# Performance work log

Hardware: AMD Instinct MI355X
Metric: run time of the kernel (lower is better)

Reference implementation:

```python
import jax, jax.numpy as jnp
import numpy as np

B = 4; RESO = 64; VIT = 16; PAD = 0.1; TRI_C = 64; IMG_C = 1280
INNER = 128; OUT_C = 64; HEADS = 8; NIMG = 5
N_TRI = 3 * RESO * RESO  # 12288 triplane locations


def pos_enc(d_model, length):
    pos = jnp.arange(length, dtype=jnp.float32)[:, None]
    div = jnp.exp(jnp.arange(0, d_model, 2, dtype=jnp.float32) * (-np.log(10000.0) / d_model))
    pe = jnp.zeros((length, d_model), jnp.float32)
    pe = pe.at[:, 0::2].set(jnp.sin(pos * div)).at[:, 1::2].set(jnp.cos(pos * div))
    return pe


def triplane_coords():
    ar = jnp.arange(RESO, dtype=jnp.float32)
    A, Bm = jnp.meshgrid(ar, ar, indexing='xy')  # matches torch indexing='xy'
    half = jnp.full_like(A, (RESO - 1) / 2.0)
    xz = jnp.stack([A, half, Bm], -1)
    xy = jnp.stack([A, Bm, half], -1)
    yz = jnp.stack([half, A, Bm], -1)
    c = jnp.concatenate([xz, xy, yz], 0).reshape(-1, 3)
    c = c / (RESO - 1)
    return (c - 0.5) * 2.0 * (1.0 + PAD + 1e-05)  # [N_TRI, 3]


def trilinear_sample(vol, grid):
    # vol [B,C,D,H,W]; grid [B,M,3] in [-1,1] as (x->W, y->H, z->D); align_corners=True
    Bv, C, D, H, W = vol.shape
    gx, gy, gz = grid[..., 0], grid[..., 1], grid[..., 2]
    ix = (gx + 1.0) * 0.5 * (W - 1)
    iy = (gy + 1.0) * 0.5 * (H - 1)
    iz = (gz + 1.0) * 0.5 * (D - 1)
    x0 = jnp.floor(ix); y0 = jnp.floor(iy); z0 = jnp.floor(iz)
    wx = ix - x0; wy = iy - y0; wz = iz - z0
    x0i = jnp.clip(x0.astype(jnp.int32), 0, W - 1); x1i = jnp.clip(x0i + 1, 0, W - 1)
    y0i = jnp.clip(y0.astype(jnp.int32), 0, H - 1); y1i = jnp.clip(y0i + 1, 0, H - 1)
    z0i = jnp.clip(z0.astype(jnp.int32), 0, D - 1); z1i = jnp.clip(z0i + 1, 0, D - 1)
    vf = vol.reshape(Bv, C, D * H * W)
    def g(zi, yi, xi):
        idx = (zi * H + yi) * W + xi  # [B,M]
        return jnp.take_along_axis(vf, idx[:, None, :], axis=2)  # [B,C,M]
    out = 0.0
    for zi, wz_ in ((z0i, 1.0 - wz), (z1i, wz)):
        for yi, wy_ in ((y0i, 1.0 - wy), (y1i, wy)):
            for xi, wx_ in ((x0i, 1.0 - wx), (x1i, wx)):
                out = out + g(zi, yi, xi) * (wz_ * wy_ * wx_)[:, None, :]
    return out  # [B,C,M]


def _forward(triplane_feat, image_feat, proj_mat, k_w, k_b, q_w, q_b, v_w, v_b,
             in_w, in_b, out_w, out_b, conv_w, conv_b, valid_frames):
    Bb, n_img = image_feat.shape[0], image_feat.shape[1]
    img = image_feat[:, :, 1:, :]  # drop CLS -> [B,n,256,1280]
    pe_img = pos_enc(INNER, VIT * VIT)  # [256,128]
    kimg = img @ k_w.T + k_b + pe_img
    vimg = img @ v_w.T + v_b + pe_img
    kv = jnp.concatenate([kimg, vimg], -1)  # [B,n,256,2E]
    vol = kv.reshape(Bb, n_img, VIT, VIT, 2 * INNER).transpose(0, 4, 1, 2, 3)  # [B,2E,D,H,W]

    coords = triplane_coords()
    homo = jnp.concatenate([coords, jnp.ones((N_TRI, 1), jnp.float32)], -1)  # [N,4]
    cin = jnp.einsum('nc,bjkc->bjnk', homo, proj_mat)  # == homo @ proj^T
    x = cin[..., 0] / cin[..., 2] / (224.0 - 1)
    y = cin[..., 1] / cin[..., 2] / (224.0 - 1)
    xy = (jnp.stack([x, y], -1) - 0.5) * 2.0
    gi = (jnp.arange(n_img, dtype=jnp.float32) / (n_img - 1) - 0.5) * 2.0
    gi = jnp.broadcast_to(gi[None, :, None, None], (Bb, n_img, N_TRI, 1))
    grid = jnp.clip(jnp.concatenate([xy, gi], -1), -1.0, 1.0)  # [B,n,N,3]

    samp = trilinear_sample(vol, grid.reshape(Bb, n_img * N_TRI, 3))
    samp = samp.reshape(Bb, 2 * INNER, n_img, N_TRI)
    kk = samp[:, :INNER].transpose(0, 3, 2, 1)  # [B,N,n,E]
    vv = samp[:, INNER:].transpose(0, 3, 2, 1)

    tq = triplane_feat.reshape(Bb, TRI_C, N_TRI).transpose(0, 2, 1)  # b (h w) c
    q = tq @ q_w.T + q_b + pos_enc(INNER, N_TRI)

    E, dh = INNER, INNER // HEADS
    Wq, Wk, Wv = in_w[:E], in_w[E:2 * E], in_w[2 * E:]
    bq, bk, bv = in_b[:E], in_b[E:2 * E], in_b[2 * E:]
    qp = (q @ Wq.T + bq).reshape(Bb, N_TRI, HEADS, dh)
    kp = (kk @ Wk.T + bk).reshape(Bb, N_TRI, n_img, HEADS, dh)
    vp = (vv @ Wv.T + bv).reshape(Bb, N_TRI, n_img, HEADS, dh)
    scores = jnp.einsum('bnhd,bnjhd->bnhj', qp, kp) / np.sqrt(dh).astype(np.float32)
    attn = jax.nn.softmax(scores, axis=-1)
    o = jnp.einsum('bnhj,bnjhd->bnhd', attn, vp).reshape(Bb, N_TRI, E)
    o = o @ out_w.T + out_b  # [B,N,E]

    t = o.transpose(0, 2, 1).reshape(Bb, E, 3 * RESO, RESO)
    return jnp.einsum('bchw,oc->bohw', t, conv_w) + conv_b[None, :, None, None]


def setup_inputs() -> dict:
    key = jax.random.key(0)
    ks = jax.random.split(key, 16)
    s = 0.02
    pm = jax.random.normal(ks[2], (B, NIMG, 4, 4), jnp.float32)
    proj = pm * 30.0  # pixel-scale projection rows
    zrow = jnp.concatenate([pm[..., 2, :3] * 0.05, 3.0 + 0.5 * jnp.abs(pm[..., 2, 3:4])], -1)
    proj_mat = proj.at[..., 2, :].set(zrow)  # positive depth, safe division
    return {
        'triplane_feat': jax.random.normal(ks[0], (B, TRI_C, 3 * RESO, RESO), jnp.float32),
        'image_feat': jax.random.normal(ks[1], (B, NIMG, VIT * VIT + 1, IMG_C), jnp.float32),
        'proj_mat': proj_mat,
        'valid_frames': jnp.ones((B, NIMG), jnp.int32),
        'k_w': jax.random.normal(ks[3], (INNER, IMG_C), jnp.float32) * s,
        'k_b': jnp.zeros((INNER,), jnp.float32),
        'q_w': jax.random.normal(ks[4], (INNER, TRI_C), jnp.float32) * s,
        'q_b': jnp.zeros((INNER,), jnp.float32),
        'v_w': jax.random.normal(ks[5], (INNER, IMG_C), jnp.float32) * s,
        'v_b': jnp.zeros((INNER,), jnp.float32),
        'in_w': jax.random.normal(ks[6], (3 * INNER, INNER), jnp.float32) * s,
        'in_b': jnp.zeros((3 * INNER,), jnp.float32),
        'out_w': jax.random.normal(ks[7], (INNER, INNER), jnp.float32) * s,
        'out_b': jnp.zeros((INNER,), jnp.float32),
        'conv_w': jax.random.normal(ks[8], (OUT_C, INNER), jnp.float32) * s,
        'conv_b': jnp.zeros((OUT_C,), jnp.float32),
    }


def reference(triplane_feat, image_feat, proj_mat, valid_frames, k_w, k_b, q_w, q_b,
              v_w, v_b, in_w, in_b, out_w, out_b, conv_w, conv_b):
    return _forward(triplane_feat, image_feat, proj_mat, k_w, k_b, q_w, q_b, v_w, v_b,
                    in_w, in_b, out_w, out_b, conv_w, conv_b, valid_frames)
```

## Files before the change

kernel.cpp:

```cpp
#include <hip/hip_runtime.h>
#include <math.h>

#define NTRI 12288

#define OFF_WT    0u
#define OFF_PEKV  327680u
#define OFF_CQWT  393216u
#define OFF_PEQ   401408u
#define OFF_W2T   1974272u
#define OFF_B2    1982464u
#define OFF_INWT  1982528u
#define OFF_KVPV  2031680u
#define OFF_GTAB  3342400u

typedef short short8 __attribute__((ext_vector_type(8)));
typedef float f32x4 __attribute__((ext_vector_type(4)));

__device__ __forceinline__ unsigned short f2bf(float f) {
  unsigned u = __float_as_uint(f);
  return (unsigned short)((u + 0x7fff + ((u >> 16) & 1)) >> 16);
}
__device__ __forceinline__ float bflo(unsigned u) {
  return __uint_as_float(u << 16);
}
__device__ __forceinline__ float bfhi(unsigned u) {
  return __uint_as_float(u & 0xffff0000u);
}

__global__ __launch_bounds__(256) void k_inwT(const float* __restrict__ in_w,
                                              float* __restrict__ inwT) {
  int idx = blockIdx.x * 256 + threadIdx.x;
  int r = idx >> 7, m = idx & 127;
  inwT[m * 384 + r] = in_w[idx];
}

__global__ __launch_bounds__(256) void k_pre(const float* __restrict__ inwT,
    const float* __restrict__ k_w, const float* __restrict__ v_w,
    const float* __restrict__ k_b, const float* __restrict__ v_b,
    const float* __restrict__ in_b, const float* __restrict__ q_w,
    const float* __restrict__ q_b, const float* __restrict__ conv_w,
    const float* __restrict__ out_w, const float* __restrict__ out_b,
    const float* __restrict__ conv_b, const float* __restrict__ proj,
    unsigned short* __restrict__ wTc, float* __restrict__ pekv,
    float* __restrict__ cqwT, float* __restrict__ peq,
    float* __restrict__ w2t, float* __restrict__ b2,
    float4* __restrict__ gtab) {
  __shared__ float spe8[8][128];
  int bb = blockIdx.x;
  int t = threadIdx.x;

  if (bb < 1280) {
    int i = bb, c = t;
    const float* src = (c < 128) ? k_w : v_w;
    float acc = 0.f;
    for (int m = 0; m < 128; ++m)
      acc += inwT[m * 384 + 128 + c] * src[m * 1280 + i];
    wTc[(size_t)c * 1280 + i] = f2bf(acc);
  } else if (bb < 1536) {
    int p = bb - 1280;
    if (t < 128) {
      float dv = (float)exp(-(double)(t & ~1) * (9.210340371976184 / 128.0));
      float arg = (float)p * dv;
      spe8[0][t] = (t & 1) ? cosf(arg) : sinf(arg);
    }
    __syncthreads();
    const float* bias = (t < 128) ? k_b : v_b;
    float acc = 0.f;
    for (int m = 0; m < 128; ++m)
      acc += inwT[m * 384 + 128 + t] * (bias[m] + spe8[0][m]);
    pekv[p * 256 + t] = acc + in_b[128 + t];
  } else if (bb < 1568) {
    int idx = (bb - 1536) * 256 + t;
    int k = idx >> 7, c = idx & 127;
    float acc = 0.f;
    for (int m = 0; m < 128; ++m)
      acc += inwT[m * 384 + c] * q_w[m * 64 + k];
    cqwT[idx] = acc;
  } else if (bb < 3104) {
    int n8 = (bb - 1568) * 8;
    for (int it = 0; it < 4; ++it) {
      int e = it * 256 + t;
      int nn = e >> 7, m = e & 127;
      float dv = (float)exp(-(double)(m & ~1) * (9.210340371976184 / 128.0));
      float arg = (float)(n8 + nn) * dv;
      spe8[nn][m] = q_b[m] + ((m & 1) ? cosf(arg) : sinf(arg));
    }
    __syncthreads();
    int c = t & 127, z = t >> 7;
    float a0 = 0, a1 = 0, a2 = 0, a3 = 0;
    for (int m = 0; m < 128; ++m) {
      float w = inwT[m * 384 + c];
      a0 += w * spe8[z * 4 + 0][m];
      a1 += w * spe8[z * 4 + 1][m];
      a2 += w * spe8[z * 4 + 2][m];
      a3 += w * spe8[z * 4 + 3][m];
    }
    float bbv = in_b[c];
    peq[(n8 + z * 4 + 0) * 128 + c] = a0 + bbv;
    peq[(n8 + z * 4 + 1) * 128 + c] = a1 + bbv;
    peq[(n8 + z * 4 + 2) * 128 + c] = a2 + bbv;
    peq[(n8 + z * 4 + 3) * 128 + c] = a3 + bbv;
  } else if (bb < 3137) {
    int idx = (bb - 3104) * 256 + t;
    if (idx < 8192) {
      int c = idx >> 6, oc = idx & 63;
      float acc = 0.f;
      for (int m = 0; m < 128; ++m)
        acc += conv_w[oc * 128 + m] * out_w[m * 128 + c];
      w2t[c * 64 + oc] = acc;
    } else if (idx < 8256) {
      int oc = idx - 8192;
      float acc = 0.f;
      for (int m = 0; m < 128; ++m)
        acc += conv_w[oc * 128 + m] * out_b[m];
      b2[oc] = acc + conv_b[oc];
    }
  } else {
    int idx = (bb - 3137) * 256 + t;
    int n = idx % NTRI;
    int bj = idx / NTRI;
    int plane = n >> 12, rem = n & 4095;
    float fa = (float)(rem & 63), fb = (float)(rem >> 6);
    float cx, cy, cz;
    if (plane == 0)      { cx = fa;    cy = 31.5f; cz = fb; }
    else if (plane == 1) { cx = fa;    cy = fb;    cz = 31.5f; }
    else                 { cx = 31.5f; cy = fa;    cz = fb; }
    const float s2 = 2.20002f;
    cx = (cx / 63.0f - 0.5f) * s2;
    cy = (cy / 63.0f - 0.5f) * s2;
    cz = (cz / 63.0f - 0.5f) * s2;
    const float* P = &proj[bj * 16];
    float d0 = cx * P[0] + cy * P[1] + cz * P[2] + P[3];
    float d1 = cx * P[4] + cy * P[5] + cz * P[6] + P[7];
    float d2 = cx * P[8] + cy * P[9] + cz * P[10] + P[11];
    float x = d0 / d2 / 223.0f;
    float y = d1 / d2 / 223.0f;
    float gx = fminf(fmaxf((x - 0.5f) * 2.0f, -1.0f), 1.0f);
    float gy = fminf(fmaxf((y - 0.5f) * 2.0f, -1.0f), 1.0f);
    float ix = (gx + 1.0f) * 7.5f, iy = (gy + 1.0f) * 7.5f;
    float fx = floorf(ix), fy = floorf(iy);
    float wx = ix - fx, wy = iy - fy;
    int x0 = (int)fx; x0 = x0 < 0 ? 0 : (x0 > 15 ? 15 : x0);
    int y0 = (int)fy; y0 = y0 < 0 ? 0 : (y0 > 15 ? 15 : y0);
    int x1 = x0 + 1 > 15 ? 15 : x0 + 1;
    int y1 = y0 + 1 > 15 ? 15 : y0 + 1;
    int pack = x0 | (x1 << 8) | (y0 << 16) | (y1 << 24);
    gtab[idx] = make_float4(wx, wy, __int_as_float(pack), 0.f);
  }
}

#define LDA 72
__global__ __launch_bounds__(256) void k_kv(const float* __restrict__ img,
    const unsigned short* __restrict__ wTc, const float* __restrict__ pekv,
    unsigned short* __restrict__ kv16) {
  __shared__ unsigned short sA[32 * LDA];
  __shared__ unsigned short sB[64 * LDA];
  int t = threadIdx.x;
  int gm = blockIdx.x >> 2;
  int gn = blockIdx.x & 3;
  int r0 = gm * 32, c0 = gn * 64;
  int lane = t & 63, w = t >> 6;
  int wm = w & 1, wn = w >> 1;
  int lrow = lane & 15, quad = lane >> 4;
  int srow = t >> 3, schunk = t & 7;
  int bj = gm >> 3;
  f32x4 acc0 = {0,0,0,0}, acc1 = {0,0,0,0};

  for (int kt = 0; kt < 20; ++kt) {
    int k0 = kt * 64;
    __syncthreads();
    {
      const float4* s = (const float4*)&img[(size_t)(r0 + srow + bj + 1) * 1280 + k0 + schunk * 8];
      float4 v0 = s[0], v1 = s[1];
      short8 av;
      av[0] = (short)f2bf(v0.x); av[1] = (short)f2bf(v0.y);
      av[2] = (short)f2bf(v0.z); av[3] = (short)f2bf(v0.w);
      av[4] = (short)f2bf(v1.x); av[5] = (short)f2bf(v1.y);
      av[6] = (short)f2bf(v1.z); av[7] = (short)f2bf(v1.w);
      *(short8*)&sA[srow * LDA + schunk * 8] = av;
      *(short8*)&sB[srow * LDA + schunk * 8] =
          *(const short8*)&wTc[(size_t)(c0 + srow) * 1280 + k0 + schunk * 8];
      *(short8*)&sB[(srow + 32) * LDA + schunk * 8] =
          *(const short8*)&wTc[(size_t)(c0 + srow + 32) * 1280 + k0 + schunk * 8];
    }
    __syncthreads();
#pragma unroll
    for (int kk = 0; kk < 2; ++kk) {
      int kof = kk * 32 + quad * 8;
      short8 a  = *(const short8*)&sA[(wm * 16 + lrow) * LDA + kof];
      short8 b0 = *(const short8*)&sB[(wn * 32 + lrow) * LDA + kof];
      short8 b1 = *(const short8*)&sB[(wn * 32 + 16 + lrow) * LDA + kof];
      acc0 = __builtin_amdgcn_mfma_f32_16x16x32_bf16(a, b0, acc0, 0, 0, 0);
      acc1 = __builtin_amdgcn_mfma_f32_16x16x32_bf16(a, b1, acc1, 0, 0, 0);
    }
  }
  f32x4 accs[2] = {acc0, acc1};
#pragma unroll
  for (int ni = 0; ni < 2; ++ni)
#pragma unroll
    for (int r = 0; r < 4; ++r) {
      int grow = r0 + wm * 16 + quad * 4 + r;
      int gcol = c0 + wn * 32 + ni * 16 + lrow;
      kv16[(size_t)grow * 256 + gcol] =
          f2bf(accs[ni][r] + pekv[(grow & 255) * 256 + gcol]);
    }
}

__global__ __launch_bounds__(256, 2) void k_main(const float* __restrict__ tri,
    const float* __restrict__ cqwT, const float* __restrict__ peq,
    const float* __restrict__ w2t, const float* __restrict__ b2,
    const unsigned short* __restrict__ kv16, const float4* __restrict__ gtab,
    float* __restrict__ outp) {
  __shared__ float sQP[32 * 132];
  __shared__ float sBuf[32 * 132];
  float* sTQ = sBuf;
  float* sO2 = sBuf;
  int t = threadIdx.x;
  int lane = t & 63, w = t >> 6;
  int b = blockIdx.x / 384;
  int n0 = (blockIdx.x % 384) * 32;

  for (int it = 0; it < 8; ++it) {
    int e = it * 256 + t;
    int k = e >> 5, pt = e & 31;
    sTQ[k * 36 + pt] = tri[(size_t)(b * 64 + k) * NTRI + n0 + pt];
  }
  __syncthreads();

  {
    int c4 = (t & 31) * 4;
    int p4 = (t >> 5) * 4;
    const float* cw = cqwT + c4;
    float4 A0 = {0,0,0,0}, A1 = {0,0,0,0}, A2 = {0,0,0,0}, A3 = {0,0,0,0};
#pragma unroll 4
    for (int k = 0; k < 64; ++k) {
      float4 wv = *(const float4*)(cw + k * 128);
      float4 aq = *(const float4*)&sTQ[k * 36 + p4];
      A0.x += aq.x * wv.x; A0.y += aq.x * wv.y; A0.z += aq.x * wv.z; A0.w += aq.x * wv.w;
      A1.x += aq.y * wv.x; A1.y += aq.y * wv.y; A1.z += aq.y * wv.z; A1.w += aq.y * wv.w;
      A2.x += aq.z * wv.x; A2.y += aq.z * wv.y; A2.z += aq.z * wv.z; A2.w += aq.z * wv.w;
      A3.x += aq.w * wv.x; A3.y += aq.w * wv.y; A3.z += aq.w * wv.z; A3.w += aq.w * wv.w;
    }
    float4 acc[4] = {A0, A1, A2, A3};
#pragma unroll
    for (int pp = 0; pp < 4; ++pp) {
      float4 pe = *(const float4*)&peq[(size_t)(n0 + p4 + pp) * 128 + c4];
      float4 r;
      r.x = acc[pp].x + pe.x; r.y = acc[pp].y + pe.y;
      r.z = acc[pp].z + pe.z; r.w = acc[pp].w + pe.w;
      *(float4*)&sQP[(p4 + pp) * 132 + c4] = r;
    }
  }
  __syncthreads();

  {
    int sub = lane & 31, half = lane >> 5, c4 = sub * 4;
    const unsigned short* Vb = kv16 + (size_t)b * 5 * 65536;
    const float4* gbase = &gtab[(size_t)(b * 5) * NTRI];
    for (int s = 0; s < 4; ++s) {
      int pt = s * 8 + w * 2 + half;
      int n = n0 + pt;
      float4 qp4 = *(const float4*)&sQP[pt * 132 + c4];
      float4 gp[5];
#pragma unroll
      for (int j = 0; j < 5; ++j) gp[j] = gbase[(size_t)j * NTRI + n];
      float4 vst[5];
      float sc[5];
#pragma unroll
      for (int j = 0; j < 5; ++j) {
        int pack = __float_as_int(gp[j].z);
        int x0 = pack & 255, x1 = (pack >> 8) & 255;
        int y0 = (pack >> 16) & 255, y1 = (pack >> 24) & 255;
        float wx = gp[j].x, wy = gp[j].y;
        const unsigned short* r0 = Vb + j * 65536 + y0 * 4096;
        const unsigned short* r1 = Vb + j * 65536 + y1 * 4096;
        int i0 = x0 * 256 + c4, i1 = x1 * 256 + c4;
        uint2 K00 = *(const uint2*)(r0 + i0), K01 = *(const uint2*)(r0 + i1);
        uint2 K10 = *(const uint2*)(r1 + i0), K11 = *(const uint2*)(r1 + i1);
        uint2 V00 = *(const uint2*)(r0 + i0 + 128), V01 = *(const uint2*)(r0 + i1 + 128);
        uint2 V10 = *(const uint2*)(r1 + i0 + 128), V11 = *(const uint2*)(r1 + i1 + 128);
        float w00 = (1.f - wx) * (1.f - wy), w01 = wx * (1.f - wy);
        float w10 = (1.f - wx) * wy, w11 = wx * wy;
        float4 kc, vc;
        kc.x = bflo(K00.x) * w00 + bflo(K01.x) * w01 + bflo(K10.x) * w10 + bflo(K11.x) * w11;
        kc.y = bfhi(K00.x) * w00 + bfhi(K01.x) * w01 + bfhi(K10.x) * w10 + bfhi(K11.x) * w11;
        kc.z = bflo(K00.y) * w00 + bflo(K01.y) * w01 + bflo(K10.y) * w10 + bflo(K11.y) * w11;
        kc.w = bfhi(K00.y) * w00 + bfhi(K01.y) * w01 + bfhi(K10.y) * w10 + bfhi(K11.y) * w11;
        vc.x = bflo(V00.x) * w00 + bflo(V01.x) * w01 + bflo(V10.x) * w10 + bflo(V11.x) * w11;
        vc.y = bfhi(V00.x) * w00 + bfhi(V01.x) * w01 + bfhi(V10.x) * w10 + bfhi(V11.x) * w11;
        vc.z = bflo(V00.y) * w00 + bflo(V01.y) * w01 + bflo(V10.y) * w10 + bflo(V11.y) * w11;
        vc.w = bfhi(V00.y) * w00 + bfhi(V01.y) * w01 + bfhi(V10.y) * w10 + bfhi(V11.y) * w11;
        vst[j] = vc;
        float pa = qp4.x * kc.x + qp4.y * kc.y + qp4.z * kc.z + qp4.w * kc.w;
        pa += __shfl_xor(pa, 1);
        pa += __shfl_xor(pa, 2);
        sc[j] = pa * 0.25f;
      }
      float mx = fmaxf(fmaxf(fmaxf(sc[0], sc[1]), fmaxf(sc[2], sc[3])), sc[4]);
      float e0 = expf(sc[0] - mx), e1 = expf(sc[1] - mx), e2 = expf(sc[2] - mx);
      float e3 = expf(sc[3] - mx), e4 = expf(sc[4] - mx);
      float inv = 1.0f / (e0 + e1 + e2 + e3 + e4);
      float4 oa;
      oa.x = (e0 * vst[0].x + e1 * vst[1].x + e2 * vst[2].x + e3 * vst[3].x + e4 * vst[4].x) * inv;
      oa.y = (e0 * vst[0].y + e1 * vst[1].y + e2 * vst[2].y + e3 * vst[3].y + e4 * vst[4].y) * inv;
      oa.z = (e0 * vst[0].z + e1 * vst[1].z + e2 * vst[2].z + e3 * vst[3].z + e4 * vst[4].z) * inv;
      oa.w = (e0 * vst[0].w + e1 * vst[1].w + e2 * vst[2].w + e3 * vst[3].w + e4 * vst[4].w) * inv;
      *(float4*)&sO2[pt * 132 + c4] = oa;
    }
  }
  __syncthreads();

  {
    int oc4 = (t & 15) * 4;
    int pg = t >> 4;
    float f00 = 0, f01 = 0, f02 = 0, f03 = 0;
    float f10 = 0, f11 = 0, f12 = 0, f13 = 0;
    const float* o0 = &sO2[(pg * 2) * 132];
    const float* o1 = &sO2[(pg * 2 + 1) * 132];
#pragma unroll 8
    for (int cc = 0; cc < 128; ++cc) {
      float4 wv = *(const float4*)&w2t[cc * 64 + oc4];
      float ax = o0[cc], ay = o1[cc];
      f00 += ax * wv.x; f01 += ax * wv.y; f02 += ax * wv.z; f03 += ax * wv.w;
      f10 += ay * wv.x; f11 += ay * wv.y; f12 += ay * wv.z; f13 += ay * wv.w;
    }
    float4 bb = *(const float4*)&b2[oc4];
    int p0 = pg * 2, p1 = pg * 2 + 1;
    sQP[(oc4 + 0) * 33 + p0] = f00 + bb.x; sQP[(oc4 + 0) * 33 + p1] = f10 + bb.x;
    sQP[(oc4 + 1) * 33 + p0] = f01 + bb.y; sQP[(oc4 + 1) * 33 + p1] = f11 + bb.y;
    sQP[(oc4 + 2) * 33 + p0] = f02 + bb.z; sQP[(oc4 + 2) * 33 + p1] = f12 + bb.z;
    sQP[(oc4 + 3) * 33 + p0] = f03 + bb.w; sQP[(oc4 + 3) * 33 + p1] = f13 + bb.w;
  }
  __syncthreads();

  for (int it = 0; it < 8; ++it) {
    int e = it * 256 + t;
    int oc = e >> 5, pt = e & 31;
    outp[(size_t)(b * 64 + oc) * NTRI + n0 + pt] = sQP[oc * 33 + pt];
  }
}

extern "C" void kernel_launch(void* const* d_in, const int* in_sizes, int n_in,
                              void* d_out, int out_size, void* d_ws, size_t ws_size,
                              hipStream_t stream) {
  const float* tri    = (const float*)d_in[0];
  const float* img    = (const float*)d_in[1];
  const float* proj   = (const float*)d_in[2];
  const float* k_w    = (const float*)d_in[4];
  const float* k_b    = (const float*)d_in[5];
  const float* q_w    = (const float*)d_in[6];
  const float* q_b    = (const float*)d_in[7];
  const float* v_w    = (const float*)d_in[8];
  const float* v_b    = (const float*)d_in[9];
  const float* in_w   = (const float*)d_in[10];
  const float* in_b   = (const float*)d_in[11];
  const float* out_w  = (const float*)d_in[12];
  const float* out_b  = (const float*)d_in[13];
  const float* conv_w = (const float*)d_in[14];
  const float* conv_b = (const float*)d_in[15];
  float* ws = (float*)d_ws;
  unsigned short* wTc  = (unsigned short*)(ws + OFF_WT);
  float* pekv = ws + OFF_PEKV;
  float* cqwT = ws + OFF_CQWT;
  float* peq  = ws + OFF_PEQ;
  float* w2t  = ws + OFF_W2T;
  float* b2   = ws + OFF_B2;
  float* inwT = ws + OFF_INWT;
  unsigned short* kv16 = (unsigned short*)(ws + OFF_KVPV);
  float* gtab = ws + OFF_GTAB;
  float* outp = (float*)d_out;

  k_inwT<<<192, 256, 0, stream>>>(in_w, inwT);
  k_pre<<<4097, 256, 0, stream>>>(inwT, k_w, v_w, k_b, v_b, in_b, q_w, q_b,
                                  conv_w, out_w, out_b, conv_b, proj,
                                  wTc, pekv, cqwT, peq, w2t, b2, (float4*)gtab);
  k_kv<<<640, 256, 0, stream>>>(img, wTc, pekv, kv16);
  k_main<<<1536, 256, 0, stream>>>(tri, cqwT, peq, w2t, b2, kv16,
                                   (const float4*)gtab, outp);
}
```

Baseline: 222.9 us.

## Drop in_w transpose kernel, read rows directly, and prefetch k_kv tiles

Removes the separate in_w transpose kernel and launch. The weight-folding branches of k_pre now read in_w rows directly as float4, and the k_w/v_w columns are staged through shared memory. The positional-encoding exp moves from double to fast float __expf. k_kv now issues global loads for the next K tile before the MFMA loop, which overlaps memory latency with compute at the cost of extra registers. The precision of the encoding constants changes slightly.

```diff
diff --git a/kernel.cpp b/kernel.cpp
--- a/kernel.cpp
+++ b/kernel.cpp
@@ -9,7 +9,6 @@
 #define OFF_PEQ   401408u
 #define OFF_W2T   1974272u
 #define OFF_B2    1982464u
-#define OFF_INWT  1982528u
 #define OFF_KVPV  2031680u
 #define OFF_GTAB  3342400u
 
@@ -27,14 +26,7 @@
   return __uint_as_float(u & 0xffff0000u);
 }
 
-__global__ __launch_bounds__(256) void k_inwT(const float* __restrict__ in_w,
-                                              float* __restrict__ inwT) {
-  int idx = blockIdx.x * 256 + threadIdx.x;
-  int r = idx >> 7, m = idx & 127;
-  inwT[m * 384 + r] = in_w[idx];
-}
-
-__global__ __launch_bounds__(256) void k_pre(const float* __restrict__ inwT,
+__global__ __launch_bounds__(256) void k_pre(const float* __restrict__ in_w,
     const float* __restrict__ k_w, const float* __restrict__ v_w,
     const float* __restrict__ k_b, const float* __restrict__ v_b,
     const float* __restrict__ in_b, const float* __restrict__ q_w,
@@ -46,50 +38,70 @@
     float* __restrict__ w2t, float* __restrict__ b2,
     float4* __restrict__ gtab) {
   __shared__ float spe8[8][128];
+  __shared__ float skv[256];
   int bb = blockIdx.x;
   int t = threadIdx.x;
 
   if (bb < 1280) {
     int i = bb, c = t;
-    const float* src = (c < 128) ? k_w : v_w;
+    if (t < 128) skv[t] = k_w[(size_t)t * 1280 + i];
+    else         skv[t] = v_w[(size_t)(t - 128) * 1280 + i];
+    __syncthreads();
+    const float* wrow = in_w + (size_t)(128 + c) * 128;
+    const float* sp = (c < 128) ? skv : (skv + 128);
     float acc = 0.f;
-    for (int m = 0; m < 128; ++m)
-      acc += inwT[m * 384 + 128 + c] * src[m * 1280 + i];
+#pragma unroll 8
+    for (int m = 0; m < 128; m += 4) {
+      float4 wv = *(const float4*)(wrow + m);
+      acc += wv.x * sp[m] + wv.y * sp[m + 1] + wv.z * sp[m + 2] + wv.w * sp[m + 3];
+    }
     wTc[(size_t)c * 1280 + i] = f2bf(acc);
   } else if (bb < 1536) {
     int p = bb - 1280;
     if (t < 128) {
-      float dv = (float)exp(-(double)(t & ~1) * (9.210340371976184 / 128.0));
+      float dv = __expf(-(float)(t & ~1) * (9.210340371976184f / 128.0f));
       float arg = (float)p * dv;
       spe8[0][t] = (t & 1) ? cosf(arg) : sinf(arg);
     }
     __syncthreads();
     const float* bias = (t < 128) ? k_b : v_b;
+    const float* wrow = in_w + (size_t)(128 + t) * 128;
     float acc = 0.f;
-    for (int m = 0; m < 128; ++m)
-      acc += inwT[m * 384 + 128 + t] * (bias[m] + spe8[0][m]);
+#pragma unroll 8
+    for (int m = 0; m < 128; m += 4) {
+      float4 wv = *(const float4*)(wrow + m);
+      acc += wv.x * (bias[m] + spe8[0][m]) + wv.y * (bias[m + 1] + spe8[0][m + 1]) +
+             wv.z * (bias[m + 2] + spe8[0][m + 2]) + wv.w * (bias[m + 3] + spe8[0][m + 3]);
+    }
     pekv[p * 256 + t] = acc + in_b[128 + t];
   } else if (bb < 1568) {
     int idx = (bb - 1536) * 256 + t;
     int k = idx >> 7, c = idx & 127;
+    const float* wrow = in_w + (size_t)c * 128;
     float acc = 0.f;
-    for (int m = 0; m < 128; ++m)
-      acc += inwT[m * 384 + c] * q_w[m * 64 + k];
+#pragma unroll 8
+    for (int m = 0; m < 128; m += 4) {
+      float4 wv = *(const float4*)(wrow + m);
+      acc += wv.x * q_w[m * 64 + k] + wv.y * q_w[(m + 1) * 64 + k] +
+             wv.z * q_w[(m + 2) * 64 + k] + wv.w * q_w[(m + 3) * 64 + k];
+    }
     cqwT[idx] = acc;
   } else if (bb < 3104) {
     int n8 = (bb - 1568) * 8;
     for (int it = 0; it < 4; ++it) {
       int e = it * 256 + t;
       int nn = e >> 7, m = e & 127;
-      float dv = (float)exp(-(double)(m & ~1) * (9.210340371976184 / 128.0));
+      float dv = __expf(-(float)(m & ~1) * (9.210340371976184f / 128.0f));
       float arg = (float)(n8 + nn) * dv;
       spe8[nn][m] = q_b[m] + ((m & 1) ? cosf(arg) : sinf(arg));
     }
     __syncthreads();
     int c = t & 127, z = t >> 7;
+    const float* wrow = in_w + (size_t)c * 128;
     float a0 = 0, a1 = 0, a2 = 0, a3 = 0;
+#pragma unroll 4
     for (int m = 0; m < 128; ++m) {
-      float w = inwT[m * 384 + c];
+      float w = wrow[m];
       a0 += w * spe8[z * 4 + 0][m];
       a1 += w * spe8[z * 4 + 1][m];
       a2 += w * spe8[z * 4 + 2][m];
@@ -104,9 +116,10 @@
     int idx = (bb - 3104) * 256 + t;
     if (idx < 8192) {
       int c = idx >> 6, oc = idx & 63;
+      const float* crow = conv_w + oc * 128;
       float acc = 0.f;
       for (int m = 0; m < 128; ++m)
-        acc += conv_w[oc * 128 + m] * out_w[m * 128 + c];
+        acc += crow[m] * out_w[m * 128 + c];
       w2t[c * 64 + oc] = acc;
     } else if (idx < 8256) {
       int oc = idx - 8192;
@@ -166,24 +179,31 @@
   int bj = gm >> 3;
   f32x4 acc0 = {0,0,0,0}, acc1 = {0,0,0,0};
 
+  float4 pA0, pA1;
+  short8 pB0, pB1;
+  auto issue = [&](int kt) {
+    int k0 = kt * 64;
+    const float4* s = (const float4*)&img[(size_t)(r0 + srow + bj + 1) * 1280 + k0 + schunk * 8];
+    pA0 = s[0]; pA1 = s[1];
+    pB0 = *(const short8*)&wTc[(size_t)(c0 + srow) * 1280 + k0 + schunk * 8];
+    pB1 = *(const short8*)&wTc[(size_t)(c0 + srow + 32) * 1280 + k0 + schunk * 8];
+  };
+  issue(0);
+
   for (int kt = 0; kt < 20; ++kt) {
-    int k0 = kt * 64;
     __syncthreads();
     {
-      const float4* s = (const float4*)&img[(size_t)(r0 + srow + bj + 1) * 1280 + k0 + schunk * 8];
-      float4 v0 = s[0], v1 = s[1];
       short8 av;
-      av[0] = (short)f2bf(v0.x); av[1] = (short)f2bf(v0.y);
-      av[2] = (short)f2bf(v0.z); av[3] = (short)f2bf(v0.w);
-      av[4] = (short)f2bf(v1.x); av[5] = (short)f2bf(v1.y);
-      av[6] = (short)f2bf(v1.z); av[7] = (short)f2bf(v1.w);
+      av[0] = (short)f2bf(pA0.x); av[1] = (short)f2bf(pA0.y);
+      av[2] = (short)f2bf(pA0.z); av[3] = (short)f2bf(pA0.w);
+      av[4] = (short)f2bf(pA1.x); av[5] = (short)f2bf(pA1.y);
+      av[6] = (short)f2bf(pA1.z); av[7] = (short)f2bf(pA1.w);
       *(short8*)&sA[srow * LDA + schunk * 8] = av;
-      *(short8*)&sB[srow * LDA + schunk * 8] =
-          *(const short8*)&wTc[(size_t)(c0 + srow) * 1280 + k0 + schunk * 8];
-      *(short8*)&sB[(srow + 32) * LDA + schunk * 8] =
-          *(const short8*)&wTc[(size_t)(c0 + srow + 32) * 1280 + k0 + schunk * 8];
-    }
-    __syncthreads();
+      *(short8*)&sB[srow * LDA + schunk * 8] = pB0;
+      *(short8*)&sB[(srow + 32) * LDA + schunk * 8] = pB1;
+    }
+    __syncthreads();
+    if (kt < 19) issue(kt + 1);
 #pragma unroll
     for (int kk = 0; kk < 2; ++kk) {
       int kof = kk * 32 + quad * 8;
@@ -365,13 +385,11 @@
   float* peq  = ws + OFF_PEQ;
   float* w2t  = ws + OFF_W2T;
   float* b2   = ws + OFF_B2;
-  float* inwT = ws + OFF_INWT;
   unsigned short* kv16 = (unsigned short*)(ws + OFF_KVPV);
   float* gtab = ws + OFF_GTAB;
   float* outp = (float*)d_out;
 
-  k_inwT<<<192, 256, 0, stream>>>(in_w, inwT);
-  k_pre<<<4097, 256, 0, stream>>>(inwT, k_w, v_w, k_b, v_b, in_b, q_w, q_b,
+  k_pre<<<4097, 256, 0, stream>>>(in_w, k_w, v_w, k_b, v_b, in_b, q_w, q_b,
                                   conv_w, out_w, out_b, conv_b, proj,
                                   wTc, pekv, cqwT, peq, w2t, b2, (float4*)gtab);
   k_kv<<<640, 256, 0, stream>>>(img, wTc, pekv, kv16);
```

Result: slower. 245.0 us (+9.9%).

## Prefetch next k-tile into registers in KV GEMM and speed up pre-kernel

Applied to the files above, without the earlier changes.

The KV projection GEMM now issues the global loads for the next k-tile into registers before running the MFMA work on the current tile, so memory latency overlaps with compute. The pre-kernel stages the strided k_w/v_w column for each block in shared memory once instead of reading it with a stride on every iteration. The double-precision exp used for the positional encoding is replaced with the fast float __expf. This raises register pressure and may slightly change the positional-encoding values.

```diff
diff --git a/kernel.cpp b/kernel.cpp
--- a/kernel.cpp
+++ b/kernel.cpp
@@ -46,20 +46,24 @@
     float* __restrict__ w2t, float* __restrict__ b2,
     float4* __restrict__ gtab) {
   __shared__ float spe8[8][128];
+  __shared__ float skv[256];
   int bb = blockIdx.x;
   int t = threadIdx.x;
 
   if (bb < 1280) {
     int i = bb, c = t;
-    const float* src = (c < 128) ? k_w : v_w;
+    if (t < 128) skv[t] = k_w[(size_t)t * 1280 + i];
+    else         skv[t] = v_w[(size_t)(t - 128) * 1280 + i];
+    __syncthreads();
+    const float* sp = (c < 128) ? skv : (skv + 128);
     float acc = 0.f;
     for (int m = 0; m < 128; ++m)
-      acc += inwT[m * 384 + 128 + c] * src[m * 1280 + i];
+      acc += inwT[m * 384 + 128 + c] * sp[m];
     wTc[(size_t)c * 1280 + i] = f2bf(acc);
   } else if (bb < 1536) {
     int p = bb - 1280;
     if (t < 128) {
-      float dv = (float)exp(-(double)(t & ~1) * (9.210340371976184 / 128.0));
+      float dv = __expf(-(float)(t & ~1) * (9.210340371976184f / 128.0f));
       float arg = (float)p * dv;
       spe8[0][t] = (t & 1) ? cosf(arg) : sinf(arg);
     }
@@ -81,7 +85,7 @@
     for (int it = 0; it < 4; ++it) {
       int e = it * 256 + t;
       int nn = e >> 7, m = e & 127;
-      float dv = (float)exp(-(double)(m & ~1) * (9.210340371976184 / 128.0));
+      float dv = __expf(-(float)(m & ~1) * (9.210340371976184f / 128.0f));
       float arg = (float)(n8 + nn) * dv;
       spe8[nn][m] = q_b[m] + ((m & 1) ? cosf(arg) : sinf(arg));
     }
@@ -166,24 +170,31 @@
   int bj = gm >> 3;
   f32x4 acc0 = {0,0,0,0}, acc1 = {0,0,0,0};
 
+  float4 pA0, pA1;
+  short8 pB0, pB1;
+  auto issue = [&](int kt) {
+    int k0 = kt * 64;
+    const float4* s = (const float4*)&img[(size_t)(r0 + srow + bj + 1) * 1280 + k0 + schunk * 8];
+    pA0 = s[0]; pA1 = s[1];
+    pB0 = *(const short8*)&wTc[(size_t)(c0 + srow) * 1280 + k0 + schunk * 8];
+    pB1 = *(const short8*)&wTc[(size_t)(c0 + srow + 32) * 1280 + k0 + schunk * 8];
+  };
+  issue(0);
+
   for (int kt = 0; kt < 20; ++kt) {
-    int k0 = kt * 64;
     __syncthreads();
     {
-      const float4* s = (const float4*)&img[(size_t)(r0 + srow + bj + 1) * 1280 + k0 + schunk * 8];
-      float4 v0 = s[0], v1 = s[1];
       short8 av;
-      av[0] = (short)f2bf(v0.x); av[1] = (short)f2bf(v0.y);
-      av[2] = (short)f2bf(v0.z); av[3] = (short)f2bf(v0.w);
-      av[4] = (short)f2bf(v1.x); av[5] = (short)f2bf(v1.y);
-      av[6] = (short)f2bf(v1.z); av[7] = (short)f2bf(v1.w);
+      av[0] = (short)f2bf(pA0.x); av[1] = (short)f2bf(pA0.y);
+      av[2] = (short)f2bf(pA0.z); av[3] = (short)f2bf(pA0.w);
+      av[4] = (short)f2bf(pA1.x); av[5] = (short)f2bf(pA1.y);
+      av[6] = (short)f2bf(pA1.z); av[7] = (short)f2bf(pA1.w);
       *(short8*)&sA[srow * LDA + schunk * 8] = av;
-      *(short8*)&sB[srow * LDA + schunk * 8] =
-          *(const short8*)&wTc[(size_t)(c0 + srow) * 1280 + k0 + schunk * 8];
-      *(short8*)&sB[(srow + 32) * LDA + schunk * 8] =
-          *(const short8*)&wTc[(size_t)(c0 + srow + 32) * 1280 + k0 + schunk * 8];
-    }
-    __syncthreads();
+      *(short8*)&sB[srow * LDA + schunk * 8] = pB0;
+      *(short8*)&sB[(srow + 32) * LDA + schunk * 8] = pB1;
+    }
+    __syncthreads();
+    if (kt < 19) issue(kt + 1);
 #pragma unroll
     for (int kk = 0; kk < 2; ++kk) {
       int kof = kk * 32 + quad * 8;
```

Result: faster. 217.6 us (-2.4%).
